# Kernel optimization log

Measured on AMD Instinct MI355X. Metric: run time of the kernel, lower is better.

Reference implementation:

```python
import jax, jax.numpy as jnp
import numpy as np

C, I, O = 32, 1024, 1024
B, T = 64, 512


def setup_inputs() -> dict:
    key = jax.random.key(0)
    kx, kc, kw, kb = jax.random.split(key, 4)
    x = jax.random.normal(kx, (B, T, I), dtype=jnp.float32)
    cat_ids = jax.random.randint(kc, (B,), 0, C)
    W = 0.02 * jax.random.normal(kw, (C, I, O), dtype=jnp.float32)
    b = jnp.zeros((C, O), dtype=jnp.float32)
    return {"x": x, "cat_ids": cat_ids, "W": W, "b": b}


def reference(x, cat_ids, W, b):
    # Per-category affine: y[b] = x[b] @ W[cat_ids[b]] + b[cat_ids[b]]
    selected_W = W[cat_ids]            # [B, I, O] (gathered per batch element)
    selected_b = b[cat_ids]            # [B, O]
    if x.ndim == 2:
        return jnp.einsum('bi,bio->bo', x, selected_W) + selected_b
    return jnp.einsum('bti,bio->bto', x, selected_W) + selected_b[:, None, :]
```

## Files before the change

### kernel.cpp

```cpp
#include <hip/hip_runtime.h>
#include <hip/hip_bf16.h>
#include <stdint.h>

#define CATS  32
#define DI    1024
#define DO    1024
#define NB    64
#define ST    512

typedef float  f32x4  __attribute__((ext_vector_type(4)));
typedef short  bf16x8 __attribute__((ext_vector_type(8)));

__device__ __forceinline__ unsigned short f2bf(float f) {
    union { float f; unsigned int u; } v;
    v.f = f;
    unsigned int r = v.u + 0x7FFFu + ((v.u >> 16) & 1u);
    return (unsigned short)(r >> 16);
}

__global__ __launch_bounds__(256) void wt_transpose_kernel(
        const float* __restrict__ W, unsigned short* __restrict__ Wt) {
    __shared__ float tile[64 * 65];
    const int c  = blockIdx.z;
    const int i0 = blockIdx.y * 64;
    const int o0 = blockIdx.x * 64;
    const float* Wc = W + (size_t)c * DI * DO;
    const int tid = threadIdx.x;

    const int f  = tid & 15;
    const int r0 = tid >> 4;
    #pragma unroll
    for (int rr = 0; rr < 4; ++rr) {
        const int r = r0 + rr * 16;
        const f32x4 v = *(const f32x4*)(Wc + (size_t)(i0 + r) * DO + (o0 + 4 * f));
        #pragma unroll
        for (int j = 0; j < 4; ++j)
            tile[r * 65 + 4 * f + j] = v[j];
    }
    __syncthreads();

    const int g   = tid & 7;
    const int ol0 = tid >> 3;
    unsigned short* WtC = Wt + (size_t)c * DO * DI;
    #pragma unroll
    for (int oo = 0; oo < 2; ++oo) {
        const int ol = ol0 + oo * 32;
        unsigned int w[4];
        #pragma unroll
        for (int j = 0; j < 4; ++j) {
            const unsigned short lo = f2bf(tile[(8 * g + 2 * j + 0) * 65 + ol]);
            const unsigned short hi = f2bf(tile[(8 * g + 2 * j + 1) * 65 + ol]);
            w[j] = (unsigned int)lo | ((unsigned int)hi << 16);
        }
        uint4 pk;
        pk.x = w[0]; pk.y = w[1]; pk.z = w[2]; pk.w = w[3];
        *(uint4*)(WtC + (size_t)(o0 + ol) * DI + (i0 + 8 * g)) = pk;
    }
}

#define BM 128
#define BN 128
#define BK 32
#define AST 40
#define KSTEPS (DI / BK)

__global__ __launch_bounds__(256) void cat_gemm_kernel(
        const float* __restrict__ x, const int* __restrict__ cat_ids,
        const unsigned short* __restrict__ Wt, const float* __restrict__ bias,
        float* __restrict__ out) {
    __shared__ __align__(16) unsigned short As[2][BM * AST];

    const int b     = blockIdx.z;
    const int mbase = blockIdx.y * BM;
    const int nbase = blockIdx.x * BN;
    const int cat   = cat_ids[b];

    const float*          xB = x  + ((size_t)b * ST + mbase) * DI;
    const unsigned short* Wc = Wt + ((size_t)cat * DO + nbase) * DI;

    const int tid  = threadIdx.x;
    const int lane = tid & 63;
    const int wv   = tid >> 6;
    const int wr   = wv >> 1;
    const int wc   = wv & 1;
    const int l15  = lane & 15;
    const int kg   = lane >> 4;

    const int sf  = tid & 7;
    const int sr0 = tid >> 3;

    const unsigned short* bptr[4];
    #pragma unroll
    for (int ni = 0; ni < 4; ++ni)
        bptr[ni] = Wc + (size_t)(wc * 64 + ni * 16 + l15) * DI + kg * 8;

    f32x4 acc[4][4];
    #pragma unroll
    for (int mi = 0; mi < 4; ++mi)
        #pragma unroll
        for (int ni = 0; ni < 4; ++ni)
            acc[mi][ni] = (f32x4){0.f, 0.f, 0.f, 0.f};

    f32x4  xg[4];
    bf16x8 bcur[4], bnxt[4];

    #pragma unroll
    for (int it = 0; it < 4; ++it)
        xg[it] = *(const f32x4*)(xB + (size_t)(sr0 + 32 * it) * DI + 4 * sf);
    #pragma unroll
    for (int ni = 0; ni < 4; ++ni)
        bcur[ni] = *(const bf16x8*)(bptr[ni]);

    #pragma unroll
    for (int it = 0; it < 4; ++it) {
        ushort4 w;
        w.x = f2bf(xg[it][0]); w.y = f2bf(xg[it][1]);
        w.z = f2bf(xg[it][2]); w.w = f2bf(xg[it][3]);
        *(ushort4*)&As[0][(sr0 + 32 * it) * AST + 4 * sf] = w;
    }
    __syncthreads();

    int buf = 0;
    #pragma unroll 1
    for (int step = 0; step < KSTEPS; ++step) {
        const int  k0n  = (step + 1) * BK;
        const bool more = (step + 1 < KSTEPS);
        if (more) {
            #pragma unroll
            for (int it = 0; it < 4; ++it)
                xg[it] = *(const f32x4*)(xB + (size_t)(sr0 + 32 * it) * DI + k0n + 4 * sf);
            #pragma unroll
            for (int ni = 0; ni < 4; ++ni)
                bnxt[ni] = *(const bf16x8*)(bptr[ni] + k0n);
        }

        bf16x8 af[4];
        #pragma unroll
        for (int mi = 0; mi < 4; ++mi)
            af[mi] = *(const bf16x8*)&As[buf][(wr * 64 + mi * 16 + l15) * AST + kg * 8];

        #pragma unroll
        for (int mi = 0; mi < 4; ++mi)
            #pragma unroll
            for (int ni = 0; ni < 4; ++ni)
                acc[mi][ni] = __builtin_amdgcn_mfma_f32_16x16x32_bf16(
                                  af[mi], bcur[ni], acc[mi][ni], 0, 0, 0);

        if (more) {
            #pragma unroll
            for (int it = 0; it < 4; ++it) {
                ushort4 w;
                w.x = f2bf(xg[it][0]); w.y = f2bf(xg[it][1]);
                w.z = f2bf(xg[it][2]); w.w = f2bf(xg[it][3]);
                *(ushort4*)&As[buf ^ 1][(sr0 + 32 * it) * AST + 4 * sf] = w;
            }
            #pragma unroll
            for (int ni = 0; ni < 4; ++ni)
                bcur[ni] = bnxt[ni];
        }
        __syncthreads();
        buf ^= 1;
    }

    float bs[4];
    #pragma unroll
    for (int ni = 0; ni < 4; ++ni)
        bs[ni] = bias[cat * DO + nbase + wc * 64 + ni * 16 + l15];

    #pragma unroll
    for (int mi = 0; mi < 4; ++mi) {
        const int rowb = mbase + wr * 64 + mi * 16 + kg * 4;
        #pragma unroll
        for (int r = 0; r < 4; ++r) {
            float* orow = out + ((size_t)b * ST + rowb + r) * DO
                              + nbase + wc * 64 + l15;
            #pragma unroll
            for (int ni = 0; ni < 4; ++ni)
                orow[ni * 16] = acc[mi][ni][r] + bs[ni];
        }
    }
}

__global__ __launch_bounds__(256) void naive_kernel(
        const float* __restrict__ x, const int* __restrict__ cat_ids,
        const float* __restrict__ W, const float* __restrict__ bias,
        float* __restrict__ out) {
    const int bt = blockIdx.x;
    const int b  = bt >> 9;
    const int t  = bt & 511;
    const int cat = cat_ids[b];
    const float* xr = x + ((size_t)b * ST + t) * DI;
    const float* Wc = W + (size_t)cat * DI * DO;
    const int o = threadIdx.x;
    float a0 = bias[cat * DO + o];
    float a1 = bias[cat * DO + o + 256];
    float a2 = bias[cat * DO + o + 512];
    float a3 = bias[cat * DO + o + 768];
    for (int i = 0; i < DI; ++i) {
        const float xv = xr[i];
        const float* wrow = Wc + (size_t)i * DO;
        a0 += xv * wrow[o];
        a1 += xv * wrow[o + 256];
        a2 += xv * wrow[o + 512];
        a3 += xv * wrow[o + 768];
    }
    float* orow = out + ((size_t)b * ST + t) * DO;
    orow[o] = a0; orow[o + 256] = a1; orow[o + 512] = a2; orow[o + 768] = a3;
}

extern "C" void kernel_launch(void* const* d_in, const int* in_sizes, int n_in,
                              void* d_out, int out_size, void* d_ws, size_t ws_size,
                              hipStream_t stream) {
    const float* x    = (const float*)d_in[0];
    const int*   cats = (const int*)d_in[1];
    const float* W    = (const float*)d_in[2];
    const float* bias = (const float*)d_in[3];
    float*       out  = (float*)d_out;

    const size_t wt_bytes = (size_t)CATS * DI * DO * sizeof(unsigned short);
    if (ws_size >= wt_bytes) {
        unsigned short* Wt = (unsigned short*)d_ws;
        wt_transpose_kernel<<<dim3(DO / 64, DI / 64, CATS), 256, 0, stream>>>(W, Wt);
        cat_gemm_kernel<<<dim3(DO / BN, ST / BM, NB), 256, 0, stream>>>(x, cats, Wt, bias, out);
    } else {
        naive_kernel<<<NB * ST, 256, 0, stream>>>(x, cats, W, bias, out);
    }
}
```

Measured before the change: 500.6 us.

## Pre-convert x to bf16 and drop LDS staging with register double-buffered MFMA

Adds a separate pass that converts x to bf16 in workspace, then rewrites the GEMM to load A and B fragments straight from global memory into registers. The shared-memory tile and per-step barriers go away, and two register buffers are alternated across the fully unrolled K loop. Tiles change to 64 rows by 256 columns, with each wave owning 64 columns. The cost is an extra pass over x (read fp32, write bf16). Without LDS, A rows are reloaded by all four waves and fetched with uncoalesced strided row reads.

```diff
diff --git a/kernel.cpp b/kernel.cpp
--- a/kernel.cpp
+++ b/kernel.cpp
@@ -52,47 +52,50 @@
             const unsigned short hi = f2bf(tile[(8 * g + 2 * j + 1) * 65 + ol]);
             w[j] = (unsigned int)lo | ((unsigned int)hi << 16);
         }
-        uint4 pk;
-        pk.x = w[0]; pk.y = w[1]; pk.z = w[2]; pk.w = w[3];
+        uint4 pk; pk.x = w[0]; pk.y = w[1]; pk.z = w[2]; pk.w = w[3];
         *(uint4*)(WtC + (size_t)(o0 + ol) * DI + (i0 + 8 * g)) = pk;
     }
 }
 
-#define BM 128
-#define BN 128
-#define BK 32
-#define AST 40
-#define KSTEPS (DI / BK)
-
+__global__ __launch_bounds__(256) void x_convert_kernel(
+        const float* __restrict__ x, unsigned short* __restrict__ xb) {
+    const size_t i = ((size_t)blockIdx.x * 256 + threadIdx.x) * 8;
+    const f32x4 v0 = *(const f32x4*)(x + i);
+    const f32x4 v1 = *(const f32x4*)(x + i + 4);
+    uint4 pk;
+    pk.x = (unsigned int)f2bf(v0[0]) | ((unsigned int)f2bf(v0[1]) << 16);
+    pk.y = (unsigned int)f2bf(v0[2]) | ((unsigned int)f2bf(v0[3]) << 16);
+    pk.z = (unsigned int)f2bf(v1[0]) | ((unsigned int)f2bf(v1[1]) << 16);
+    pk.w = (unsigned int)f2bf(v1[2]) | ((unsigned int)f2bf(v1[3]) << 16);
+    *(uint4*)(xb + i) = pk;
+}
+
+template<int XB>
 __global__ __launch_bounds__(256) void cat_gemm_kernel(
-        const float* __restrict__ x, const int* __restrict__ cat_ids,
+        const unsigned short* __restrict__ xb, const float* __restrict__ xf,
+        const int* __restrict__ cat_ids,
         const unsigned short* __restrict__ Wt, const float* __restrict__ bias,
         float* __restrict__ out) {
-    __shared__ __align__(16) unsigned short As[2][BM * AST];
-
-    const int b     = blockIdx.z;
-    const int mbase = blockIdx.y * BM;
-    const int nbase = blockIdx.x * BN;
-    const int cat   = cat_ids[b];
-
-    const float*          xB = x  + ((size_t)b * ST + mbase) * DI;
-    const unsigned short* Wc = Wt + ((size_t)cat * DO + nbase) * DI;
+    const int b    = blockIdx.z;
+    const int mblk = blockIdx.y;
+    const int nblk = blockIdx.x;
+    const int cat  = cat_ids[b];
 
     const int tid  = threadIdx.x;
     const int lane = tid & 63;
     const int wv   = tid >> 6;
-    const int wr   = wv >> 1;
-    const int wc   = wv & 1;
     const int l15  = lane & 15;
     const int kg   = lane >> 4;
 
-    const int sf  = tid & 7;
-    const int sr0 = tid >> 3;
-
-    const unsigned short* bptr[4];
-    #pragma unroll
-    for (int ni = 0; ni < 4; ++ni)
-        bptr[ni] = Wc + (size_t)(wc * 64 + ni * 16 + l15) * DI + kg * 8;
+    const int mrow = mblk * 64 + l15;
+    const int ncol = nblk * 256 + wv * 64 + l15;
+
+    const unsigned short* ap_h =
+        XB ? xb + (size_t)(b * ST + mrow) * DI + kg * 8 : nullptr;
+    const float* ap_f =
+        XB ? nullptr : xf + (size_t)(b * ST + mrow) * DI + kg * 8;
+    const unsigned short* bp =
+        Wt + ((size_t)cat * DO + ncol) * DI + kg * 8;
 
     f32x4 acc[4][4];
     #pragma unroll
@@ -101,79 +104,73 @@
         for (int ni = 0; ni < 4; ++ni)
             acc[mi][ni] = (f32x4){0.f, 0.f, 0.f, 0.f};
 
-    f32x4  xg[4];
-    bf16x8 bcur[4], bnxt[4];
-
-    #pragma unroll
-    for (int it = 0; it < 4; ++it)
-        xg[it] = *(const f32x4*)(xB + (size_t)(sr0 + 32 * it) * DI + 4 * sf);
-    #pragma unroll
-    for (int ni = 0; ni < 4; ++ni)
-        bcur[ni] = *(const bf16x8*)(bptr[ni]);
-
-    #pragma unroll
-    for (int it = 0; it < 4; ++it) {
-        ushort4 w;
-        w.x = f2bf(xg[it][0]); w.y = f2bf(xg[it][1]);
-        w.z = f2bf(xg[it][2]); w.w = f2bf(xg[it][3]);
-        *(ushort4*)&As[0][(sr0 + 32 * it) * AST + 4 * sf] = w;
-    }
-    __syncthreads();
-
-    int buf = 0;
-    #pragma unroll 1
-    for (int step = 0; step < KSTEPS; ++step) {
-        const int  k0n  = (step + 1) * BK;
-        const bool more = (step + 1 < KSTEPS);
-        if (more) {
-            #pragma unroll
-            for (int it = 0; it < 4; ++it)
-                xg[it] = *(const f32x4*)(xB + (size_t)(sr0 + 32 * it) * DI + k0n + 4 * sf);
-            #pragma unroll
-            for (int ni = 0; ni < 4; ++ni)
-                bnxt[ni] = *(const bf16x8*)(bptr[ni] + k0n);
-        }
-
-        bf16x8 af[4];
-        #pragma unroll
-        for (int mi = 0; mi < 4; ++mi)
-            af[mi] = *(const bf16x8*)&As[buf][(wr * 64 + mi * 16 + l15) * AST + kg * 8];
-
+    #define LOAD_A(dst, k0)                                                    \
+        do {                                                                   \
+            if (XB) {                                                          \
+                _Pragma("unroll")                                              \
+                for (int mi = 0; mi < 4; ++mi)                                 \
+                    dst[mi] = *(const bf16x8*)(ap_h + (size_t)mi * 16 * DI + (k0)); \
+            } else {                                                           \
+                _Pragma("unroll")                                              \
+                for (int mi = 0; mi < 4; ++mi) {                               \
+                    const f32x4 u0 = *(const f32x4*)(ap_f + (size_t)mi * 16 * DI + (k0));     \
+                    const f32x4 u1 = *(const f32x4*)(ap_f + (size_t)mi * 16 * DI + (k0) + 4); \
+                    bf16x8 r;                                                  \
+                    r[0] = (short)f2bf(u0[0]); r[1] = (short)f2bf(u0[1]);      \
+                    r[2] = (short)f2bf(u0[2]); r[3] = (short)f2bf(u0[3]);      \
+                    r[4] = (short)f2bf(u1[0]); r[5] = (short)f2bf(u1[1]);      \
+                    r[6] = (short)f2bf(u1[2]); r[7] = (short)f2bf(u1[3]);      \
+                    dst[mi] = r;                                               \
+                }                                                              \
+            }                                                                  \
+        } while (0)
+
+    #define LOAD_B(dst, k0)                                                    \
+        do {                                                                   \
+            _Pragma("unroll")                                                  \
+            for (int ni = 0; ni < 4; ++ni)                                     \
+                dst[ni] = *(const bf16x8*)(bp + (size_t)ni * 16 * DI + (k0));  \
+        } while (0)
+
+    bf16x8 a0[4], b0[4], a1[4], b1[4];
+    LOAD_A(a0, 0);
+    LOAD_B(b0, 0);
+
+    #pragma unroll
+    for (int k0 = 0; k0 < DI; k0 += 64) {
+        LOAD_A(a1, k0 + 32);
+        LOAD_B(b1, k0 + 32);
         #pragma unroll
         for (int mi = 0; mi < 4; ++mi)
             #pragma unroll
             for (int ni = 0; ni < 4; ++ni)
                 acc[mi][ni] = __builtin_amdgcn_mfma_f32_16x16x32_bf16(
-                                  af[mi], bcur[ni], acc[mi][ni], 0, 0, 0);
-
-        if (more) {
-            #pragma unroll
-            for (int it = 0; it < 4; ++it) {
-                ushort4 w;
-                w.x = f2bf(xg[it][0]); w.y = f2bf(xg[it][1]);
-                w.z = f2bf(xg[it][2]); w.w = f2bf(xg[it][3]);
-                *(ushort4*)&As[buf ^ 1][(sr0 + 32 * it) * AST + 4 * sf] = w;
-            }
+                                  a0[mi], b0[ni], acc[mi][ni], 0, 0, 0);
+        if (k0 + 64 < DI) {
+            LOAD_A(a0, k0 + 64);
+            LOAD_B(b0, k0 + 64);
+        }
+        #pragma unroll
+        for (int mi = 0; mi < 4; ++mi)
             #pragma unroll
             for (int ni = 0; ni < 4; ++ni)
-                bcur[ni] = bnxt[ni];
-        }
-        __syncthreads();
-        buf ^= 1;
-    }
+                acc[mi][ni] = __builtin_amdgcn_mfma_f32_16x16x32_bf16(
+                                  a1[mi], b1[ni], acc[mi][ni], 0, 0, 0);
+    }
+    #undef LOAD_A
+    #undef LOAD_B
 
     float bs[4];
     #pragma unroll
     for (int ni = 0; ni < 4; ++ni)
-        bs[ni] = bias[cat * DO + nbase + wc * 64 + ni * 16 + l15];
+        bs[ni] = bias[(size_t)cat * DO + ncol + ni * 16];
 
     #pragma unroll
     for (int mi = 0; mi < 4; ++mi) {
-        const int rowb = mbase + wr * 64 + mi * 16 + kg * 4;
+        const int rowb = mblk * 64 + mi * 16 + kg * 4;
         #pragma unroll
         for (int r = 0; r < 4; ++r) {
-            float* orow = out + ((size_t)b * ST + rowb + r) * DO
-                              + nbase + wc * 64 + l15;
+            float* orow = out + (size_t)(b * ST + rowb + r) * DO + ncol;
             #pragma unroll
             for (int ni = 0; ni < 4; ++ni)
                 orow[ni * 16] = acc[mi][ni][r] + bs[ni];
@@ -218,10 +215,20 @@
     float*       out  = (float*)d_out;
 
     const size_t wt_bytes = (size_t)CATS * DI * DO * sizeof(unsigned short);
-    if (ws_size >= wt_bytes) {
+    const size_t xb_bytes = (size_t)NB * ST * DI * sizeof(unsigned short);
+
+    if (ws_size >= wt_bytes + xb_bytes) {
+        unsigned short* Wt = (unsigned short*)d_ws;
+        unsigned short* xb = (unsigned short*)((char*)d_ws + wt_bytes);
+        wt_transpose_kernel<<<dim3(DO / 64, DI / 64, CATS), 256, 0, stream>>>(W, Wt);
+        x_convert_kernel<<<(NB * ST * DI) / (256 * 8), 256, 0, stream>>>(x, xb);
+        cat_gemm_kernel<1><<<dim3(DO / 256, ST / 64, NB), 256, 0, stream>>>(
+            xb, nullptr, cats, Wt, bias, out);
+    } else if (ws_size >= wt_bytes) {
         unsigned short* Wt = (unsigned short*)d_ws;
         wt_transpose_kernel<<<dim3(DO / 64, DI / 64, CATS), 256, 0, stream>>>(W, Wt);
-        cat_gemm_kernel<<<dim3(DO / BN, ST / BM, NB), 256, 0, stream>>>(x, cats, Wt, bias, out);
+        cat_gemm_kernel<0><<<dim3(DO / 256, ST / 64, NB), 256, 0, stream>>>(
+            nullptr, x, cats, Wt, bias, out);
     } else {
         naive_kernel<<<NB * ST, 256, 0, stream>>>(x, cats, W, bias, out);
     }
```

Result: slower. 554.6 us (+10.8%).

## Pre-convert x to bf16 and stage both GEMM operands via direct global-to-LDS loads

Applied to the files above, without the earlier changes.

Adds a separate pass that converts x to bf16 in workspace. The GEMM now stages both A and B tiles into LDS using global_load_lds with an XOR-swizzled chunk layout, replacing the old path: in-loop fp32 loads plus conversion for A, and direct-to-register global loads for B. The weight transpose tile also grows to 128 rows per block. The aim is to remove conversion work and register staging from the GEMM inner loop and cut global-load latency. The cost is an extra full pass over x, and the workspace requirement doubles, which risks falling back to the naive kernel if the workspace is too small.

```diff
diff --git a/kernel.cpp b/kernel.cpp
--- a/kernel.cpp
+++ b/kernel.cpp
@@ -20,9 +20,9 @@
 
 __global__ __launch_bounds__(256) void wt_transpose_kernel(
         const float* __restrict__ W, unsigned short* __restrict__ Wt) {
-    __shared__ float tile[64 * 65];
+    __shared__ float tile[128 * 65];
     const int c  = blockIdx.z;
-    const int i0 = blockIdx.y * 64;
+    const int i0 = blockIdx.y * 128;
     const int o0 = blockIdx.x * 64;
     const float* Wc = W + (size_t)c * DI * DO;
     const int tid = threadIdx.x;
@@ -30,7 +30,7 @@
     const int f  = tid & 15;
     const int r0 = tid >> 4;
     #pragma unroll
-    for (int rr = 0; rr < 4; ++rr) {
+    for (int rr = 0; rr < 8; ++rr) {
         const int r = r0 + rr * 16;
         const f32x4 v = *(const f32x4*)(Wc + (size_t)(i0 + r) * DO + (o0 + 4 * f));
         #pragma unroll
@@ -39,12 +39,12 @@
     }
     __syncthreads();
 
-    const int g   = tid & 7;
-    const int ol0 = tid >> 3;
+    const int g   = tid & 15;
+    const int ol0 = tid >> 4;
     unsigned short* WtC = Wt + (size_t)c * DO * DI;
     #pragma unroll
-    for (int oo = 0; oo < 2; ++oo) {
-        const int ol = ol0 + oo * 32;
+    for (int oo = 0; oo < 4; ++oo) {
+        const int ol = ol0 + oo * 16;
         unsigned int w[4];
         #pragma unroll
         for (int j = 0; j < 4; ++j) {
@@ -52,47 +52,55 @@
             const unsigned short hi = f2bf(tile[(8 * g + 2 * j + 1) * 65 + ol]);
             w[j] = (unsigned int)lo | ((unsigned int)hi << 16);
         }
-        uint4 pk;
-        pk.x = w[0]; pk.y = w[1]; pk.z = w[2]; pk.w = w[3];
+        uint4 pk; pk.x = w[0]; pk.y = w[1]; pk.z = w[2]; pk.w = w[3];
         *(uint4*)(WtC + (size_t)(o0 + ol) * DI + (i0 + 8 * g)) = pk;
     }
+}
+
+__global__ __launch_bounds__(256) void x_convert_kernel(
+        const float* __restrict__ x, unsigned short* __restrict__ xb) {
+    const size_t i = ((size_t)blockIdx.x * 256 + threadIdx.x) * 8;
+    const f32x4 v0 = *(const f32x4*)(x + i);
+    const f32x4 v1 = *(const f32x4*)(x + i + 4);
+    uint4 pk;
+    pk.x = (unsigned int)f2bf(v0[0]) | ((unsigned int)f2bf(v0[1]) << 16);
+    pk.y = (unsigned int)f2bf(v0[2]) | ((unsigned int)f2bf(v0[3]) << 16);
+    pk.z = (unsigned int)f2bf(v1[0]) | ((unsigned int)f2bf(v1[1]) << 16);
+    pk.w = (unsigned int)f2bf(v1[2]) | ((unsigned int)f2bf(v1[3]) << 16);
+    *(uint4*)(xb + i) = pk;
 }
 
 #define BM 128
 #define BN 128
 #define BK 32
-#define AST 40
-#define KSTEPS (DI / BK)
 
 __global__ __launch_bounds__(256) void cat_gemm_kernel(
-        const float* __restrict__ x, const int* __restrict__ cat_ids,
+        const unsigned short* __restrict__ xb, const int* __restrict__ cat_ids,
         const unsigned short* __restrict__ Wt, const float* __restrict__ bias,
         float* __restrict__ out) {
-    __shared__ __align__(16) unsigned short As[2][BM * AST];
+    __shared__ __align__(16) unsigned short As[2][BM * BK];
+    __shared__ __align__(16) unsigned short Bs[2][BN * BK];
 
     const int b     = blockIdx.z;
     const int mbase = blockIdx.y * BM;
     const int nbase = blockIdx.x * BN;
     const int cat   = cat_ids[b];
 
-    const float*          xB = x  + ((size_t)b * ST + mbase) * DI;
-    const unsigned short* Wc = Wt + ((size_t)cat * DO + nbase) * DI;
-
     const int tid  = threadIdx.x;
     const int lane = tid & 63;
-    const int wv   = tid >> 6;
-    const int wr   = wv >> 1;
-    const int wc   = wv & 1;
+    const int w    = tid >> 6;
+    const int wr   = w >> 1;
+    const int wc   = w & 1;
     const int l15  = lane & 15;
     const int kg   = lane >> 4;
 
-    const int sf  = tid & 7;
-    const int sr0 = tid >> 3;
-
-    const unsigned short* bptr[4];
-    #pragma unroll
-    for (int ni = 0; ni < 4; ++ni)
-        bptr[ni] = Wc + (size_t)(wc * 64 + ni * 16 + l15) * DI + kg * 8;
+    const int sr     = lane >> 2;
+    const int schunk = (lane & 3) ^ ((lane >> 3) & 3);
+
+    const unsigned short* gA = xb + (size_t)(b * ST + mbase) * DI;
+    const unsigned short* gB = Wt + ((size_t)cat * DO + nbase) * DI;
+
+    const int koff = (kg ^ ((l15 >> 1) & 3)) * 8;
 
     f32x4 acc[4][4];
     #pragma unroll
@@ -101,78 +109,70 @@
         for (int ni = 0; ni < 4; ++ni)
             acc[mi][ni] = (f32x4){0.f, 0.f, 0.f, 0.f};
 
-    f32x4  xg[4];
-    bf16x8 bcur[4], bnxt[4];
-
-    #pragma unroll
-    for (int it = 0; it < 4; ++it)
-        xg[it] = *(const f32x4*)(xB + (size_t)(sr0 + 32 * it) * DI + 4 * sf);
-    #pragma unroll
-    for (int ni = 0; ni < 4; ++ni)
-        bcur[ni] = *(const bf16x8*)(bptr[ni]);
-
-    #pragma unroll
-    for (int it = 0; it < 4; ++it) {
-        ushort4 w;
-        w.x = f2bf(xg[it][0]); w.y = f2bf(xg[it][1]);
-        w.z = f2bf(xg[it][2]); w.w = f2bf(xg[it][3]);
-        *(ushort4*)&As[0][(sr0 + 32 * it) * AST + 4 * sf] = w;
-    }
+    #define STAGE(bufi, k0)                                                          \
+        do {                                                                         \
+            _Pragma("unroll")                                                        \
+            for (int q = 0; q < 2; ++q) {                                            \
+                const int row = w * 32 + q * 16 + sr;                                \
+                __builtin_amdgcn_global_load_lds(                                    \
+                    (const __attribute__((address_space(1))) void*)                  \
+                        (gA + (size_t)row * DI + (k0) + schunk * 8),                 \
+                    (__attribute__((address_space(3))) void*)                        \
+                        &As[bufi][(w * 32 + q * 16) * BK],                           \
+                    16, 0, 0);                                                       \
+                __builtin_amdgcn_global_load_lds(                                    \
+                    (const __attribute__((address_space(1))) void*)                  \
+                        (gB + (size_t)row * DI + (k0) + schunk * 8),                 \
+                    (__attribute__((address_space(3))) void*)                        \
+                        &Bs[bufi][(w * 32 + q * 16) * BK],                           \
+                    16, 0, 0);                                                       \
+            }                                                                        \
+        } while (0)
+
+    STAGE(0, 0);
     __syncthreads();
 
     int buf = 0;
     #pragma unroll 1
-    for (int step = 0; step < KSTEPS; ++step) {
-        const int  k0n  = (step + 1) * BK;
-        const bool more = (step + 1 < KSTEPS);
-        if (more) {
-            #pragma unroll
-            for (int it = 0; it < 4; ++it)
-                xg[it] = *(const f32x4*)(xB + (size_t)(sr0 + 32 * it) * DI + k0n + 4 * sf);
-            #pragma unroll
-            for (int ni = 0; ni < 4; ++ni)
-                bnxt[ni] = *(const bf16x8*)(bptr[ni] + k0n);
-        }
-
-        bf16x8 af[4];
-        #pragma unroll
-        for (int mi = 0; mi < 4; ++mi)
-            af[mi] = *(const bf16x8*)&As[buf][(wr * 64 + mi * 16 + l15) * AST + kg * 8];
+    for (int step = 0; step < DI / BK; ++step) {
+        if (step + 1 < DI / BK)
+            STAGE(buf ^ 1, (step + 1) * BK);
+
+        bf16x8 af[4], bf[4];
+        #pragma unroll
+        for (int mi = 0; mi < 4; ++mi) {
+            const int m = wr * 64 + mi * 16 + l15;
+            af[mi] = *(const bf16x8*)&As[buf][m * BK + koff];
+        }
+        #pragma unroll
+        for (int ni = 0; ni < 4; ++ni) {
+            const int n = wc * 64 + ni * 16 + l15;
+            bf[ni] = *(const bf16x8*)&Bs[buf][n * BK + koff];
+        }
 
         #pragma unroll
         for (int mi = 0; mi < 4; ++mi)
             #pragma unroll
             for (int ni = 0; ni < 4; ++ni)
                 acc[mi][ni] = __builtin_amdgcn_mfma_f32_16x16x32_bf16(
-                                  af[mi], bcur[ni], acc[mi][ni], 0, 0, 0);
-
-        if (more) {
-            #pragma unroll
-            for (int it = 0; it < 4; ++it) {
-                ushort4 w;
-                w.x = f2bf(xg[it][0]); w.y = f2bf(xg[it][1]);
-                w.z = f2bf(xg[it][2]); w.w = f2bf(xg[it][3]);
-                *(ushort4*)&As[buf ^ 1][(sr0 + 32 * it) * AST + 4 * sf] = w;
-            }
-            #pragma unroll
-            for (int ni = 0; ni < 4; ++ni)
-                bcur[ni] = bnxt[ni];
-        }
+                                  af[mi], bf[ni], acc[mi][ni], 0, 0, 0);
+
         __syncthreads();
         buf ^= 1;
     }
+    #undef STAGE
 
     float bs[4];
     #pragma unroll
     for (int ni = 0; ni < 4; ++ni)
-        bs[ni] = bias[cat * DO + nbase + wc * 64 + ni * 16 + l15];
+        bs[ni] = bias[(size_t)cat * DO + nbase + wc * 64 + ni * 16 + l15];
 
     #pragma unroll
     for (int mi = 0; mi < 4; ++mi) {
         const int rowb = mbase + wr * 64 + mi * 16 + kg * 4;
         #pragma unroll
         for (int r = 0; r < 4; ++r) {
-            float* orow = out + ((size_t)b * ST + rowb + r) * DO
+            float* orow = out + (size_t)(b * ST + rowb + r) * DO
                               + nbase + wc * 64 + l15;
             #pragma unroll
             for (int ni = 0; ni < 4; ++ni)
@@ -218,10 +218,15 @@
     float*       out  = (float*)d_out;
 
     const size_t wt_bytes = (size_t)CATS * DI * DO * sizeof(unsigned short);
-    if (ws_size >= wt_bytes) {
+    const size_t xb_bytes = (size_t)NB * ST * DI * sizeof(unsigned short);
+
+    if (ws_size >= wt_bytes + xb_bytes) {
         unsigned short* Wt = (unsigned short*)d_ws;
-        wt_transpose_kernel<<<dim3(DO / 64, DI / 64, CATS), 256, 0, stream>>>(W, Wt);
-        cat_gemm_kernel<<<dim3(DO / BN, ST / BM, NB), 256, 0, stream>>>(x, cats, Wt, bias, out);
+        unsigned short* xb = (unsigned short*)((char*)d_ws + wt_bytes);
+        wt_transpose_kernel<<<dim3(DO / 64, DI / 128, CATS), 256, 0, stream>>>(W, Wt);
+        x_convert_kernel<<<(NB * ST * DI) / (256 * 8), 256, 0, stream>>>(x, xb);
+        cat_gemm_kernel<<<dim3(DO / BN, ST / BM, NB), 256, 0, stream>>>(
+            xb, cats, Wt, bias, out);
     } else {
         naive_kernel<<<NB * ST, 256, 0, stream>>>(x, cats, W, bias, out);
     }
```

Result: faster. 429.8 us (-14.1%).
